# Kernel optimization log

Measured on AMD Instinct MI355X. Metric: run time of the kernel, lower is better.

The kernel has to match this reference:

```python
import jax, jax.numpy as jnp
import numpy as np
from functools import partial

TAU = 2.0
V_TH = 1.0
ALPHA = 2.0  # spikingjelly surrogate.ATan default alpha
EPS = 1e-5   # nn.LayerNorm default eps

@jax.custom_vjp
def atan_spike(v):
    # Heaviside forward; ATan surrogate gradient in bwd.
    return (v >= 0.0).astype(v.dtype)

def _atan_fwd(v):
    return atan_spike(v), v

def _atan_bwd(v, g):
    sg = (ALPHA / 2.0) / (1.0 + (jnp.pi / 2.0 * ALPHA * v) ** 2)
    return (g * sg,)

atan_spike.defvjp(_atan_fwd, _atan_bwd)

def lif_multi_step(x):
    # x: [B, T, H]; LIF with decay_input=True, v_reset=0 (hard reset), detach_reset=True.
    xt = jnp.swapaxes(x, 0, 1)  # [T, B, H]
    v0 = jnp.zeros(x.shape[:1] + x.shape[2:], dtype=x.dtype)  # reset_net per call
    def step(v, x_t):
        v = v + (x_t - v) / TAU            # charge
        s = atan_spike(v - V_TH)           # fire (surrogate grad)
        v = v * (1.0 - jax.lax.stop_gradient(s))  # hard reset to 0, detached spike
        return v, s
    _, spikes = jax.lax.scan(step, v0, xt)
    return jnp.swapaxes(spikes, 0, 1)  # [B, T, H]

def layer_norm(x, gamma, beta):
    mu = jnp.mean(x, axis=-1, keepdims=True)
    var = jnp.mean((x - mu) ** 2, axis=-1, keepdims=True)
    return (x - mu) * jax.lax.rsqrt(var + EPS) * gamma + beta

def setup_inputs() -> dict:
    key = jax.random.key(0)
    ks = jax.random.split(key, 5)
    B, T, D, H = 64, 1024, 256, 512
    x = jax.random.normal(ks[0], (B, T, D), dtype=jnp.float32)
    sc1 = 1.0 / np.sqrt(D)
    sc2 = 1.0 / np.sqrt(H)
    W1 = jax.random.uniform(ks[1], (H, D), jnp.float32, -sc1, sc1)
    b1 = jax.random.uniform(ks[2], (H,), jnp.float32, -sc1, sc1)
    W2 = jax.random.uniform(ks[3], (D, H), jnp.float32, -sc2, sc2)
    b2 = jax.random.uniform(ks[4], (D,), jnp.float32, -sc2, sc2)
    g1 = jnp.ones((H,), jnp.float32); be1 = jnp.zeros((H,), jnp.float32)
    g2 = jnp.ones((D,), jnp.float32); be2 = jnp.zeros((D,), jnp.float32)
    return {"x": x, "W1": W1, "b1": b1, "g1": g1, "be1": be1,
            "W2": W2, "b2": b2, "g2": g2, "be2": be2}

def reference(x, W1, b1, g1, be1, W2, b2, g2, be2):
    residual = x
    h = jnp.einsum('btd,hd->bth', x, W1) + b1   # fc1
    h = layer_norm(h, g1, be1)                   # norm1
    h = lif_multi_step(h)                        # lif1 (dropout = identity, eval)
    y = jnp.einsum('bth,dh->btd', h, W2) + b2    # fc2
    y = layer_norm(y, g2, be2)                   # norm2
    y = lif_multi_step(y)                        # lif2
    return residual + y
```

## Files before the change

kernel.cpp:

```cpp
#include <hip/hip_runtime.h>

typedef int v4i  __attribute__((ext_vector_type(4)));
typedef int v16i __attribute__((ext_vector_type(16)));

#define TT 1024
#define DD 256
#define HH 512
#define CB 32
#define CM (CB*TT)

__device__ __forceinline__ double shfl_xor_d(double x, int m) {
    union { double d; int u[2]; } a; a.d = x;
    a.u[0] = __shfl_xor(a.u[0], m);
    a.u[1] = __shfl_xor(a.u[1], m);
    return a.d;
}

__global__ __launch_bounds__(256) void prep_w_k(const float* __restrict__ W1,
                                                const float* __restrict__ W2,
                                                signed char* __restrict__ W1p,
                                                signed char* __restrict__ W2p) {
    int i = blockIdx.x * 256 + threadIdx.x;
    {
        double a = (double)W1[i];
        double inv = 1024.0, s = 1.0 / 1024.0;
#pragma unroll
        for (int p = 0; p < 5; ++p) {
            int d = (int)(a * inv);
            a -= d * s;
            W1p[(size_t)p * 131072 + i] = (signed char)d;
            inv *= 128.0; s *= (1.0 / 128.0);
        }
    }
    {
        double a = (double)W2[i];
        double inv = 1024.0, s = 1.0 / 1024.0;
#pragma unroll
        for (int p = 0; p < 5; ++p) {
            int d = (int)(a * inv);
            a -= d * s;
            W2p[(size_t)p * 131072 + i] = (signed char)d;
            inv *= 128.0; s *= (1.0 / 128.0);
        }
    }
}

__global__ __launch_bounds__(512, 2) void gemm1_i8(
    const float* __restrict__ X, const signed char* __restrict__ W1p,
    const float* __restrict__ b1, const float* __restrict__ g1,
    const float* __restrict__ be1, double* __restrict__ Hn) {
    __shared__ signed char Asm[5 * 8192];
    __shared__ double RS[8][32], RQ[8][32];
    __shared__ double MUs[32], IVs[32];

    const int tid = threadIdx.x;
    const int wave = tid >> 6, lane = tid & 63, lrow = lane & 31, lhalf = lane >> 5;
    const int m0 = blockIdx.x * 32;

    {
        const int r = tid >> 4;
        const int k0 = (tid & 15) * 16;
        const float* xp = X + (size_t)(m0 + r) * DD + k0;
        float xe[16];
        *(float4*)(xe + 0)  = *(const float4*)(xp + 0);
        *(float4*)(xe + 4)  = *(const float4*)(xp + 4);
        *(float4*)(xe + 8)  = *(const float4*)(xp + 8);
        *(float4*)(xe + 12) = *(const float4*)(xp + 12);
        int pk[5][4];
#pragma unroll
        for (int q = 0; q < 4; ++q)
#pragma unroll
            for (int e = 0; e < 4; ++e) {
                float a = xe[q * 4 + e];
                float inv = 8.0f, s = 0.125f;
#pragma unroll
                for (int p = 0; p < 5; ++p) {
                    int d = (int)(a * inv);
                    a -= (float)d * s;
                    int byte = (d & 255) << (8 * e);
                    if (e == 0) pk[p][q] = byte; else pk[p][q] |= byte;
                    inv *= 128.0f; s *= (1.0f / 128.0f);
                }
            }
        const int swz = k0 ^ ((r & 7) << 4);
#pragma unroll
        for (int p = 0; p < 5; ++p)
            *(v4i*)&Asm[p * 8192 + r * 256 + swz] = *(const v4i*)pk[p];
    }

    v16i acc[5][2];
#pragma unroll
    for (int g = 0; g < 5; ++g)
#pragma unroll
        for (int nt = 0; nt < 2; ++nt)
#pragma unroll
            for (int r = 0; r < 16; ++r) acc[g][nt][r] = 0;

    const signed char* bb[2];
    bb[0] = W1p + (size_t)(wave * 64 + lrow) * 256 + lhalf * 16;
    bb[1] = bb[0] + 32 * 256;

    v4i cb[2][2];
#pragma unroll
    for (int nt = 0; nt < 2; ++nt)
#pragma unroll
        for (int ks = 0; ks < 2; ++ks)
            cb[nt][ks] = *(const v4i*)(bb[nt] + ks * 32);

    __syncthreads();

    const int aswz = (lrow & 7) << 4;
#pragma unroll
    for (int j = 0; j < 5; ++j)
#pragma unroll
        for (int kk = 0; kk < 4; ++kk) {
            const int it = j * 4 + kk;
            v4i nb[2][2];
            if (it < 19) {
                const int nj = (kk == 3) ? j + 1 : j;
                const int nkk = (kk == 3) ? 0 : kk + 1;
                const size_t off = (size_t)nj * 131072 + nkk * 64;
#pragma unroll
                for (int nt = 0; nt < 2; ++nt)
#pragma unroll
                    for (int ks = 0; ks < 2; ++ks)
                        nb[nt][ks] = *(const v4i*)(bb[nt] + off + ks * 32);
            }
#pragma unroll
            for (int i = 0; i + j < 5; ++i) {
                v4i a0 = *(const v4i*)&Asm[i * 8192 + lrow * 256 +
                                           ((kk * 64 + lhalf * 16) ^ aswz)];
                v4i a1 = *(const v4i*)&Asm[i * 8192 + lrow * 256 +
                                           ((kk * 64 + 32 + lhalf * 16) ^ aswz)];
                acc[i + j][0] = __builtin_amdgcn_mfma_i32_32x32x32_i8(a0, cb[0][0], acc[i + j][0], 0, 0, 0);
                acc[i + j][0] = __builtin_amdgcn_mfma_i32_32x32x32_i8(a1, cb[0][1], acc[i + j][0], 0, 0, 0);
                acc[i + j][1] = __builtin_amdgcn_mfma_i32_32x32x32_i8(a0, cb[1][0], acc[i + j][1], 0, 0, 0);
                acc[i + j][1] = __builtin_amdgcn_mfma_i32_32x32x32_i8(a1, cb[1][1], acc[i + j][1], 0, 0, 0);
            }
#pragma unroll
            for (int nt = 0; nt < 2; ++nt)
#pragma unroll
                for (int ks = 0; ks < 2; ++ks)
                    cb[nt][ks] = nb[nt][ks];
        }

    const double scl[5] = {0x1p-13, 0x1p-20, 0x1p-27, 0x1p-34, 0x1p-41};
    double vv[2][16];
    int colc[2];
#pragma unroll
    for (int nt = 0; nt < 2; ++nt) {
        colc[nt] = wave * 64 + nt * 32 + lrow;
        double bcol = (double)b1[colc[nt]];
#pragma unroll
        for (int r = 0; r < 16; ++r) {
            double t = 0.0;
#pragma unroll
            for (int g = 0; g < 5; ++g) t = fma((double)acc[g][nt][r], scl[g], t);
            vv[nt][r] = t + bcol;
        }
    }
    double ps[16], pq[16];
#pragma unroll
    for (int r = 0; r < 16; ++r) {
        ps[r] = vv[0][r] + vv[1][r];
        pq[r] = vv[0][r] * vv[0][r] + vv[1][r] * vv[1][r];
    }
#pragma unroll
    for (int m = 1; m < 32; m <<= 1)
#pragma unroll
        for (int r = 0; r < 16; ++r) {
            ps[r] += shfl_xor_d(ps[r], m);
            pq[r] += shfl_xor_d(pq[r], m);
        }
    if (lrow == 0) {
#pragma unroll
        for (int r = 0; r < 16; ++r) {
            int rw = (r & 3) + 8 * (r >> 2) + 4 * lhalf;
            RS[wave][rw] = ps[r];
            RQ[wave][rw] = pq[r];
        }
    }
    __syncthreads();
    if (tid < 32) {
        double s = 0.0, q = 0.0;
#pragma unroll
        for (int w = 0; w < 8; ++w) { s += RS[w][tid]; q += RQ[w][tid]; }
        double mu = s * (1.0 / 512.0);
        double var = q * (1.0 / 512.0) - mu * mu;
        MUs[tid] = mu;
        IVs[tid] = 1.0 / sqrt(var + 1e-5);
    }
    __syncthreads();
#pragma unroll
    for (int nt = 0; nt < 2; ++nt) {
        int col = colc[nt];
        double gg = (double)g1[col], bb2 = (double)be1[col];
#pragma unroll
        for (int r = 0; r < 16; ++r) {
            int rw = (r & 3) + 8 * (r >> 2) + 4 * lhalf;
            double o = (vv[nt][r] - MUs[rw]) * IVs[rw] * gg + bb2;
            Hn[(size_t)(m0 + rw) * 512 + col] = o;
        }
    }
}

__global__ __launch_bounds__(512, 2) void gemm2_i8(
    const signed char* __restrict__ S, const signed char* __restrict__ W2p,
    const float* __restrict__ b2, const float* __restrict__ g2,
    const float* __restrict__ be2, double* __restrict__ Yn) {
    __shared__ signed char Asm[64 * 512];
    __shared__ double RS[4][64], RQ[4][64];
    __shared__ double MUs[64], IVs[64];

    const int tid = threadIdx.x;
    const int wave = tid >> 6, lane = tid & 63, lrow = lane & 31, lhalf = lane >> 5;
    const int wm = wave >> 2, wn = wave & 3;
    const int m0 = blockIdx.x * 64;

    {
        const int r = tid >> 3, k0 = (tid & 7) * 64;
#pragma unroll
        for (int q = 0; q < 4; ++q) {
            int k = k0 + q * 16;
            v4i v = *(const v4i*)(S + (size_t)(m0 + r) * 512 + k);
            *(v4i*)&Asm[r * 512 + (k ^ ((r & 7) << 4))] = v;
        }
    }

    v16i acc[5][2];
#pragma unroll
    for (int g = 0; g < 5; ++g)
#pragma unroll
        for (int nt = 0; nt < 2; ++nt)
#pragma unroll
            for (int r = 0; r < 16; ++r) acc[g][nt][r] = 0;

    const signed char* bb[2];
    bb[0] = W2p + (size_t)(wn * 64 + lrow) * 512 + lhalf * 16;
    bb[1] = bb[0] + 32 * 512;

    v4i cb[2][4];
#pragma unroll
    for (int nt = 0; nt < 2; ++nt)
#pragma unroll
        for (int ks = 0; ks < 4; ++ks)
            cb[nt][ks] = *(const v4i*)(bb[nt] + ks * 32);

    __syncthreads();

    const int arow = wm * 32 + lrow;
    const int aswz = (arow & 7) << 4;
#pragma unroll
    for (int j = 0; j < 5; ++j)
#pragma unroll
        for (int kk = 0; kk < 4; ++kk) {
            const int it = j * 4 + kk;
            v4i nb[2][4];
            if (it < 19) {
                const int nj = (kk == 3) ? j + 1 : j;
                const int nkk = (kk == 3) ? 0 : kk + 1;
                const size_t off = (size_t)nj * 131072 + nkk * 128;
#pragma unroll
                for (int nt = 0; nt < 2; ++nt)
#pragma unroll
                    for (int ks = 0; ks < 4; ++ks)
                        nb[nt][ks] = *(const v4i*)(bb[nt] + off + ks * 32);
            }
#pragma unroll
            for (int ks = 0; ks < 4; ++ks) {
                v4i a = *(const v4i*)&Asm[arow * 512 +
                                          ((kk * 128 + ks * 32 + lhalf * 16) ^ aswz)];
                acc[j][0] = __builtin_amdgcn_mfma_i32_32x32x32_i8(a, cb[0][ks], acc[j][0], 0, 0, 0);
                acc[j][1] = __builtin_amdgcn_mfma_i32_32x32x32_i8(a, cb[1][ks], acc[j][1], 0, 0, 0);
            }
#pragma unroll
            for (int nt = 0; nt < 2; ++nt)
#pragma unroll
                for (int ks = 0; ks < 4; ++ks)
                    cb[nt][ks] = nb[nt][ks];
        }

    const double scl[5] = {0x1p-10, 0x1p-17, 0x1p-24, 0x1p-31, 0x1p-38};
    double vv[2][16];
    int colc[2];
#pragma unroll
    for (int nt = 0; nt < 2; ++nt) {
        colc[nt] = wn * 64 + nt * 32 + lrow;
        double bcol = (double)b2[colc[nt]];
#pragma unroll
        for (int r = 0; r < 16; ++r) {
            double t = 0.0;
#pragma unroll
            for (int g = 0; g < 5; ++g) t = fma((double)acc[g][nt][r], scl[g], t);
            vv[nt][r] = t + bcol;
        }
    }
    double ps[16], pq[16];
#pragma unroll
    for (int r = 0; r < 16; ++r) {
        ps[r] = vv[0][r] + vv[1][r];
        pq[r] = vv[0][r] * vv[0][r] + vv[1][r] * vv[1][r];
    }
#pragma unroll
    for (int m = 1; m < 32; m <<= 1)
#pragma unroll
        for (int r = 0; r < 16; ++r) {
            ps[r] += shfl_xor_d(ps[r], m);
            pq[r] += shfl_xor_d(pq[r], m);
        }
    if (lrow == 0) {
#pragma unroll
        for (int r = 0; r < 16; ++r) {
            int rw = wm * 32 + (r & 3) + 8 * (r >> 2) + 4 * lhalf;
            RS[wn][rw] = ps[r];
            RQ[wn][rw] = pq[r];
        }
    }
    __syncthreads();
    if (tid < 64) {
        double s = 0.0, q = 0.0;
#pragma unroll
        for (int w = 0; w < 4; ++w) { s += RS[w][tid]; q += RQ[w][tid]; }
        double mu = s * (1.0 / 256.0);
        double var = q * (1.0 / 256.0) - mu * mu;
        MUs[tid] = mu;
        IVs[tid] = 1.0 / sqrt(var + 1e-5);
    }
    __syncthreads();
#pragma unroll
    for (int nt = 0; nt < 2; ++nt) {
        int col = colc[nt];
        double gg = (double)g2[col], bb2 = (double)be2[col];
#pragma unroll
        for (int r = 0; r < 16; ++r) {
            int rw = wm * 32 + (r & 3) + 8 * (r >> 2) + 4 * lhalf;
            double o = (vv[nt][r] - MUs[rw]) * IVs[rw] * gg + bb2;
            Yn[(size_t)(m0 + rw) * 256 + col] = o;
        }
    }
}

__global__ __launch_bounds__(64) void lif1_k(const double* __restrict__ Hn,
                                             signed char* __restrict__ S) {
    int b = blockIdx.x >> 3;
    int h = (blockIdx.x & 7) * 64 + threadIdx.x;
    const double* src = Hn + (size_t)b * TT * HH + h;
    signed char* dst = S + (size_t)b * TT * HH + h;
    double v = 0.0;
    double buf[4][16];
#pragma unroll
    for (int gg = 0; gg < 3; ++gg)
#pragma unroll
        for (int t = 0; t < 16; ++t) buf[gg][t] = src[(size_t)(gg * 16 + t) * HH];
    for (int g4 = 0; g4 < 64; g4 += 4) {
#pragma unroll
        for (int u = 0; u < 4; ++u) {
            int g = g4 + u;
            if (g + 3 < 64) {
#pragma unroll
                for (int t = 0; t < 16; ++t)
                    buf[(u + 3) & 3][t] = src[(size_t)((g + 3) * 16 + t) * HH];
            }
#pragma unroll
            for (int t = 0; t < 16; ++t) {
                v += (buf[u][t] - v) * 0.5;
                bool sp = (v >= 1.0);
                dst[(size_t)(g * 16 + t) * HH] = sp ? 1 : 0;
                if (sp) v = 0.0;
            }
        }
    }
}

__global__ __launch_bounds__(64) void lif2_k(const double* __restrict__ Yn,
                                             const float* __restrict__ X,
                                             float* __restrict__ out) {
    int b = blockIdx.x >> 2;
    int d = (blockIdx.x & 3) * 64 + threadIdx.x;
    const double* src = Yn + (size_t)b * TT * DD + d;
    const float* xs = X + (size_t)b * TT * DD + d;
    float* dst = out + (size_t)b * TT * DD + d;
    double v = 0.0;
    double bufy[4][16];
    float bufx[4][16];
#pragma unroll
    for (int gg = 0; gg < 3; ++gg)
#pragma unroll
        for (int t = 0; t < 16; ++t) {
            bufy[gg][t] = src[(size_t)(gg * 16 + t) * DD];
            bufx[gg][t] = xs[(size_t)(gg * 16 + t) * DD];
        }
    for (int g4 = 0; g4 < 64; g4 += 4) {
#pragma unroll
        for (int u = 0; u < 4; ++u) {
            int g = g4 + u;
            if (g + 3 < 64) {
#pragma unroll
                for (int t = 0; t < 16; ++t) {
                    bufy[(u + 3) & 3][t] = src[(size_t)((g + 3) * 16 + t) * DD];
                    bufx[(u + 3) & 3][t] = xs[(size_t)((g + 3) * 16 + t) * DD];
                }
            }
#pragma unroll
            for (int t = 0; t < 16; ++t) {
                v += (bufy[u][t] - v) * 0.5;
                bool sp = (v >= 1.0);
                dst[(size_t)(g * 16 + t) * DD] = bufx[u][t] + (sp ? 1.0f : 0.0f);
                if (sp) v = 0.0;
            }
        }
    }
}

extern "C" void kernel_launch(void* const* d_in, const int* in_sizes, int n_in,
                              void* d_out, int out_size, void* d_ws, size_t ws_size,
                              hipStream_t stream) {
    const float* x   = (const float*)d_in[0];
    const float* W1  = (const float*)d_in[1];
    const float* b1  = (const float*)d_in[2];
    const float* g1  = (const float*)d_in[3];
    const float* be1 = (const float*)d_in[4];
    const float* W2  = (const float*)d_in[5];
    const float* b2  = (const float*)d_in[6];
    const float* g2  = (const float*)d_in[7];
    const float* be2 = (const float*)d_in[8];
    float* out = (float*)d_out;

    char* ws = (char*)d_ws;
    signed char* W1p = (signed char*)ws;
    signed char* W2p = (signed char*)(ws + (1ull << 20));
    double*      Hn  = (double*)(ws + (2ull << 20));
    signed char* Sb  = (signed char*)(ws + (130ull << 20));
    double*      Yn  = (double*)(ws + (146ull << 20));

    prep_w_k<<<dim3(512), dim3(256), 0, stream>>>(W1, W2, W1p, W2p);

    for (int c = 0; c < 2; ++c) {
        const float* xc = x + (size_t)c * CM * DD;
        float* outc = out + (size_t)c * CM * DD;
        gemm1_i8<<<dim3(CM / 32), dim3(512), 0, stream>>>(xc, W1p, b1, g1, be1, Hn);
        lif1_k<<<dim3(CB * 8), dim3(64), 0, stream>>>(Hn, Sb);
        gemm2_i8<<<dim3(CM / 64), dim3(512), 0, stream>>>(Sb, W2p, b2, g2, be2, Yn);
        lif2_k<<<dim3(CB * 4), dim3(64), 0, stream>>>(Yn, xc, outc);
    }
}
```

Measured before the change: 693.5 us.

## Reorder int8 split-GEMM loops to use one accumulator bank and add nontemporal memory hints

Both int8 split-precision GEMMs are restructured so MFMAs are grouped by output significance level. One pair of v16i accumulators is flushed into double accumulators when each level finishes, replacing five live accumulator banks and aiming to cut VGPR/AGPR pressure. B-fragment prefetch becomes a 3-deep ring two stages ahead. Streaming loads and stores in the GEMMs and LIF kernels become nontemporal, to reduce cache pollution from single-use data. The flushes add int-to-double conversions inside the main loop, which may serialise MFMA issue.

Measured after the change: 1.112 ms. 1.6x slower.

```diff
diff --git a/kernel.cpp b/kernel.cpp
--- a/kernel.cpp
+++ b/kernel.cpp
@@ -1,7 +1,8 @@
 #include <hip/hip_runtime.h>
 
-typedef int v4i  __attribute__((ext_vector_type(4)));
-typedef int v16i __attribute__((ext_vector_type(16)));
+typedef int   v4i __attribute__((ext_vector_type(4)));
+typedef int  v16i __attribute__((ext_vector_type(16)));
+typedef float v4f __attribute__((ext_vector_type(4)));
 
 #define TT 1024
 #define DD 256
@@ -45,6 +46,14 @@
     }
 }
 
+__device__ __forceinline__ void stage1_of(int s, int& g, int& j, int& kk) {
+    if (s < 4)       { g = 0; j = s >> 2;        kk = s & 3; }
+    else if (s < 12) { g = 1; j = (s - 4) >> 2;  kk = (s - 4) & 3; }
+    else if (s < 24) { g = 2; j = (s - 12) >> 2; kk = (s - 12) & 3; }
+    else if (s < 40) { g = 3; j = (s - 24) >> 2; kk = (s - 24) & 3; }
+    else             { g = 4; j = (s - 40) >> 2; kk = (s - 40) & 3; }
+}
+
 __global__ __launch_bounds__(512, 2) void gemm1_i8(
     const float* __restrict__ X, const signed char* __restrict__ W1p,
     const float* __restrict__ b1, const float* __restrict__ g1,
@@ -62,10 +71,10 @@
         const int k0 = (tid & 15) * 16;
         const float* xp = X + (size_t)(m0 + r) * DD + k0;
         float xe[16];
-        *(float4*)(xe + 0)  = *(const float4*)(xp + 0);
-        *(float4*)(xe + 4)  = *(const float4*)(xp + 4);
-        *(float4*)(xe + 8)  = *(const float4*)(xp + 8);
-        *(float4*)(xe + 12) = *(const float4*)(xp + 12);
+        *(v4f*)(xe + 0)  = __builtin_nontemporal_load((const v4f*)(xp + 0));
+        *(v4f*)(xe + 4)  = __builtin_nontemporal_load((const v4f*)(xp + 4));
+        *(v4f*)(xe + 8)  = __builtin_nontemporal_load((const v4f*)(xp + 8));
+        *(v4f*)(xe + 12) = __builtin_nontemporal_load((const v4f*)(xp + 12));
         int pk[5][4];
 #pragma unroll
         for (int q = 0; q < 4; ++q)
@@ -88,76 +97,73 @@
             *(v4i*)&Asm[p * 8192 + r * 256 + swz] = *(const v4i*)pk[p];
     }
 
-    v16i acc[5][2];
-#pragma unroll
-    for (int g = 0; g < 5; ++g)
-#pragma unroll
-        for (int nt = 0; nt < 2; ++nt)
-#pragma unroll
-            for (int r = 0; r < 16; ++r) acc[g][nt][r] = 0;
-
     const signed char* bb[2];
     bb[0] = W1p + (size_t)(wave * 64 + lrow) * 256 + lhalf * 16;
     bb[1] = bb[0] + 32 * 256;
 
-    v4i cb[2][2];
-#pragma unroll
-    for (int nt = 0; nt < 2; ++nt)
-#pragma unroll
-        for (int ks = 0; ks < 2; ++ks)
-            cb[nt][ks] = *(const v4i*)(bb[nt] + ks * 32);
+    v16i bank[2];
+    double vv[2][16];
+#pragma unroll
+    for (int nt = 0; nt < 2; ++nt) {
+#pragma unroll
+        for (int r = 0; r < 16; ++r) { bank[nt][r] = 0; vv[nt][r] = 0.0; }
+    }
+
+    v4i bp[3][2][2];
+#pragma unroll
+    for (int s = 0; s < 2; ++s) {
+        int g, j, kk; stage1_of(s, g, j, kk);
+        const size_t off = (size_t)j * 131072 + kk * 64;
+#pragma unroll
+        for (int nt = 0; nt < 2; ++nt)
+#pragma unroll
+            for (int ks = 0; ks < 2; ++ks)
+                bp[s][nt][ks] = *(const v4i*)(bb[nt] + off + ks * 32);
+    }
 
     __syncthreads();
 
     const int aswz = (lrow & 7) << 4;
-#pragma unroll
-    for (int j = 0; j < 5; ++j)
-#pragma unroll
-        for (int kk = 0; kk < 4; ++kk) {
-            const int it = j * 4 + kk;
-            v4i nb[2][2];
-            if (it < 19) {
-                const int nj = (kk == 3) ? j + 1 : j;
-                const int nkk = (kk == 3) ? 0 : kk + 1;
-                const size_t off = (size_t)nj * 131072 + nkk * 64;
-#pragma unroll
-                for (int nt = 0; nt < 2; ++nt)
-#pragma unroll
-                    for (int ks = 0; ks < 2; ++ks)
-                        nb[nt][ks] = *(const v4i*)(bb[nt] + off + ks * 32);
-            }
-#pragma unroll
-            for (int i = 0; i + j < 5; ++i) {
-                v4i a0 = *(const v4i*)&Asm[i * 8192 + lrow * 256 +
-                                           ((kk * 64 + lhalf * 16) ^ aswz)];
-                v4i a1 = *(const v4i*)&Asm[i * 8192 + lrow * 256 +
-                                           ((kk * 64 + 32 + lhalf * 16) ^ aswz)];
-                acc[i + j][0] = __builtin_amdgcn_mfma_i32_32x32x32_i8(a0, cb[0][0], acc[i + j][0], 0, 0, 0);
-                acc[i + j][0] = __builtin_amdgcn_mfma_i32_32x32x32_i8(a1, cb[0][1], acc[i + j][0], 0, 0, 0);
-                acc[i + j][1] = __builtin_amdgcn_mfma_i32_32x32x32_i8(a0, cb[1][0], acc[i + j][1], 0, 0, 0);
-                acc[i + j][1] = __builtin_amdgcn_mfma_i32_32x32x32_i8(a1, cb[1][1], acc[i + j][1], 0, 0, 0);
-            }
+    const double scl[5] = {0x1p-13, 0x1p-20, 0x1p-27, 0x1p-34, 0x1p-41};
+#pragma unroll
+    for (int s = 0; s < 60; ++s) {
+        int g, j, kk; stage1_of(s, g, j, kk);
+        if (s + 2 < 60) {
+            int g2, j2, k2; stage1_of(s + 2, g2, j2, k2);
+            const size_t off = (size_t)j2 * 131072 + k2 * 64;
 #pragma unroll
             for (int nt = 0; nt < 2; ++nt)
 #pragma unroll
                 for (int ks = 0; ks < 2; ++ks)
-                    cb[nt][ks] = nb[nt][ks];
-        }
-
-    const double scl[5] = {0x1p-13, 0x1p-20, 0x1p-27, 0x1p-34, 0x1p-41};
-    double vv[2][16];
+                    bp[(s + 2) % 3][nt][ks] = *(const v4i*)(bb[nt] + off + ks * 32);
+        }
+        const int i = g - j;
+        v4i a0 = *(const v4i*)&Asm[i * 8192 + lrow * 256 +
+                                   ((kk * 64 + lhalf * 16) ^ aswz)];
+        v4i a1 = *(const v4i*)&Asm[i * 8192 + lrow * 256 +
+                                   ((kk * 64 + 32 + lhalf * 16) ^ aswz)];
+        bank[0] = __builtin_amdgcn_mfma_i32_32x32x32_i8(a0, bp[s % 3][0][0], bank[0], 0, 0, 0);
+        bank[0] = __builtin_amdgcn_mfma_i32_32x32x32_i8(a1, bp[s % 3][0][1], bank[0], 0, 0, 0);
+        bank[1] = __builtin_amdgcn_mfma_i32_32x32x32_i8(a0, bp[s % 3][1][0], bank[1], 0, 0, 0);
+        bank[1] = __builtin_amdgcn_mfma_i32_32x32x32_i8(a1, bp[s % 3][1][1], bank[1], 0, 0, 0);
+        if (kk == 3 && j == g) {
+#pragma unroll
+            for (int nt = 0; nt < 2; ++nt)
+#pragma unroll
+                for (int r = 0; r < 16; ++r) {
+                    vv[nt][r] = fma((double)bank[nt][r], scl[g], vv[nt][r]);
+                    bank[nt][r] = 0;
+                }
+        }
+    }
+
     int colc[2];
 #pragma unroll
     for (int nt = 0; nt < 2; ++nt) {
         colc[nt] = wave * 64 + nt * 32 + lrow;
         double bcol = (double)b1[colc[nt]];
 #pragma unroll
-        for (int r = 0; r < 16; ++r) {
-            double t = 0.0;
-#pragma unroll
-            for (int g = 0; g < 5; ++g) t = fma((double)acc[g][nt][r], scl[g], t);
-            vv[nt][r] = t + bcol;
-        }
+        for (int r = 0; r < 16; ++r) vv[nt][r] += bcol;
     }
     double ps[16], pq[16];
 #pragma unroll
@@ -199,7 +205,7 @@
         for (int r = 0; r < 16; ++r) {
             int rw = (r & 3) + 8 * (r >> 2) + 4 * lhalf;
             double o = (vv[nt][r] - MUs[rw]) * IVs[rw] * gg + bb2;
-            Hn[(size_t)(m0 + rw) * 512 + col] = o;
+            __builtin_nontemporal_store(o, &Hn[(size_t)(m0 + rw) * 512 + col]);
         }
     }
 }
@@ -222,78 +228,75 @@
 #pragma unroll
         for (int q = 0; q < 4; ++q) {
             int k = k0 + q * 16;
-            v4i v = *(const v4i*)(S + (size_t)(m0 + r) * 512 + k);
+            v4i v = __builtin_nontemporal_load(
+                (const v4i*)(S + (size_t)(m0 + r) * 512 + k));
             *(v4i*)&Asm[r * 512 + (k ^ ((r & 7) << 4))] = v;
         }
     }
-
-    v16i acc[5][2];
-#pragma unroll
-    for (int g = 0; g < 5; ++g)
-#pragma unroll
-        for (int nt = 0; nt < 2; ++nt)
-#pragma unroll
-            for (int r = 0; r < 16; ++r) acc[g][nt][r] = 0;
 
     const signed char* bb[2];
     bb[0] = W2p + (size_t)(wn * 64 + lrow) * 512 + lhalf * 16;
     bb[1] = bb[0] + 32 * 512;
 
-    v4i cb[2][4];
-#pragma unroll
-    for (int nt = 0; nt < 2; ++nt)
-#pragma unroll
-        for (int ks = 0; ks < 4; ++ks)
-            cb[nt][ks] = *(const v4i*)(bb[nt] + ks * 32);
+    v16i bank[2];
+    double vv[2][16];
+#pragma unroll
+    for (int nt = 0; nt < 2; ++nt) {
+#pragma unroll
+        for (int r = 0; r < 16; ++r) { bank[nt][r] = 0; vv[nt][r] = 0.0; }
+    }
+
+    v4i bp[3][2][2];
+#pragma unroll
+    for (int s = 0; s < 2; ++s) {
+        const size_t off = (size_t)(s >> 3) * 131072 + (s & 7) * 64;
+#pragma unroll
+        for (int nt = 0; nt < 2; ++nt)
+#pragma unroll
+            for (int ks = 0; ks < 2; ++ks)
+                bp[s][nt][ks] = *(const v4i*)(bb[nt] + off + ks * 32);
+    }
 
     __syncthreads();
 
     const int arow = wm * 32 + lrow;
     const int aswz = (arow & 7) << 4;
-#pragma unroll
-    for (int j = 0; j < 5; ++j)
-#pragma unroll
-        for (int kk = 0; kk < 4; ++kk) {
-            const int it = j * 4 + kk;
-            v4i nb[2][4];
-            if (it < 19) {
-                const int nj = (kk == 3) ? j + 1 : j;
-                const int nkk = (kk == 3) ? 0 : kk + 1;
-                const size_t off = (size_t)nj * 131072 + nkk * 128;
-#pragma unroll
-                for (int nt = 0; nt < 2; ++nt)
-#pragma unroll
-                    for (int ks = 0; ks < 4; ++ks)
-                        nb[nt][ks] = *(const v4i*)(bb[nt] + off + ks * 32);
-            }
-#pragma unroll
-            for (int ks = 0; ks < 4; ++ks) {
-                v4i a = *(const v4i*)&Asm[arow * 512 +
-                                          ((kk * 128 + ks * 32 + lhalf * 16) ^ aswz)];
-                acc[j][0] = __builtin_amdgcn_mfma_i32_32x32x32_i8(a, cb[0][ks], acc[j][0], 0, 0, 0);
-                acc[j][1] = __builtin_amdgcn_mfma_i32_32x32x32_i8(a, cb[1][ks], acc[j][1], 0, 0, 0);
-            }
+    const double scl[5] = {0x1p-10, 0x1p-17, 0x1p-24, 0x1p-31, 0x1p-38};
+#pragma unroll
+    for (int s = 0; s < 40; ++s) {
+        const int j = s >> 3, kh = s & 7;
+        if (s + 2 < 40) {
+            const size_t off = (size_t)((s + 2) >> 3) * 131072 + ((s + 2) & 7) * 64;
 #pragma unroll
             for (int nt = 0; nt < 2; ++nt)
 #pragma unroll
-                for (int ks = 0; ks < 4; ++ks)
-                    cb[nt][ks] = nb[nt][ks];
-        }
-
-    const double scl[5] = {0x1p-10, 0x1p-17, 0x1p-24, 0x1p-31, 0x1p-38};
-    double vv[2][16];
+                for (int ks = 0; ks < 2; ++ks)
+                    bp[(s + 2) % 3][nt][ks] = *(const v4i*)(bb[nt] + off + ks * 32);
+        }
+        v4i a0 = *(const v4i*)&Asm[arow * 512 + ((kh * 64 + lhalf * 16) ^ aswz)];
+        v4i a1 = *(const v4i*)&Asm[arow * 512 + ((kh * 64 + 32 + lhalf * 16) ^ aswz)];
+        bank[0] = __builtin_amdgcn_mfma_i32_32x32x32_i8(a0, bp[s % 3][0][0], bank[0], 0, 0, 0);
+        bank[0] = __builtin_amdgcn_mfma_i32_32x32x32_i8(a1, bp[s % 3][0][1], bank[0], 0, 0, 0);
+        bank[1] = __builtin_amdgcn_mfma_i32_32x32x32_i8(a0, bp[s % 3][1][0], bank[1], 0, 0, 0);
+        bank[1] = __builtin_amdgcn_mfma_i32_32x32x32_i8(a1, bp[s % 3][1][1], bank[1], 0, 0, 0);
+        if (kh == 7) {
+#pragma unroll
+            for (int nt = 0; nt < 2; ++nt)
+#pragma unroll
+                for (int r = 0; r < 16; ++r) {
+                    vv[nt][r] = fma((double)bank[nt][r], scl[j], vv[nt][r]);
+                    bank[nt][r] = 0;
+                }
+        }
+    }
+
     int colc[2];
 #pragma unroll
     for (int nt = 0; nt < 2; ++nt) {
         colc[nt] = wn * 64 + nt * 32 + lrow;
         double bcol = (double)b2[colc[nt]];
 #pragma unroll
-        for (int r = 0; r < 16; ++r) {
-            double t = 0.0;
-#pragma unroll
-            for (int g = 0; g < 5; ++g) t = fma((double)acc[g][nt][r], scl[g], t);
-            vv[nt][r] = t + bcol;
-        }
+        for (int r = 0; r < 16; ++r) vv[nt][r] += bcol;
     }
     double ps[16], pq[16];
 #pragma unroll
@@ -335,7 +338,7 @@
         for (int r = 0; r < 16; ++r) {
             int rw = wm * 32 + (r & 3) + 8 * (r >> 2) + 4 * lhalf;
             double o = (vv[nt][r] - MUs[rw]) * IVs[rw] * gg + bb2;
-            Yn[(size_t)(m0 + rw) * 256 + col] = o;
+            __builtin_nontemporal_store(o, &Yn[(size_t)(m0 + rw) * 256 + col]);
         }
     }
 }
@@ -351,7 +354,8 @@
 #pragma unroll
     for (int gg = 0; gg < 3; ++gg)
 #pragma unroll
-        for (int t = 0; t < 16; ++t) buf[gg][t] = src[(size_t)(gg * 16 + t) * HH];
+        for (int t = 0; t < 16; ++t)
+            buf[gg][t] = __builtin_nontemporal_load(&src[(size_t)(gg * 16 + t) * HH]);
     for (int g4 = 0; g4 < 64; g4 += 4) {
 #pragma unroll
         for (int u = 0; u < 4; ++u) {
@@ -359,7 +363,8 @@
             if (g + 3 < 64) {
 #pragma unroll
                 for (int t = 0; t < 16; ++t)
-                    buf[(u + 3) & 3][t] = src[(size_t)((g + 3) * 16 + t) * HH];
+                    buf[(u + 3) & 3][t] =
+                        __builtin_nontemporal_load(&src[(size_t)((g + 3) * 16 + t) * HH]);
             }
 #pragma unroll
             for (int t = 0; t < 16; ++t) {
@@ -387,8 +392,8 @@
     for (int gg = 0; gg < 3; ++gg)
 #pragma unroll
         for (int t = 0; t < 16; ++t) {
-            bufy[gg][t] = src[(size_t)(gg * 16 + t) * DD];
-            bufx[gg][t] = xs[(size_t)(gg * 16 + t) * DD];
+            bufy[gg][t] = __builtin_nontemporal_load(&src[(size_t)(gg * 16 + t) * DD]);
+            bufx[gg][t] = __builtin_nontemporal_load(&xs[(size_t)(gg * 16 + t) * DD]);
         }
     for (int g4 = 0; g4 < 64; g4 += 4) {
 #pragma unroll
@@ -397,15 +402,18 @@
             if (g + 3 < 64) {
 #pragma unroll
                 for (int t = 0; t < 16; ++t) {
-                    bufy[(u + 3) & 3][t] = src[(size_t)((g + 3) * 16 + t) * DD];
-                    bufx[(u + 3) & 3][t] = xs[(size_t)((g + 3) * 16 + t) * DD];
+                    bufy[(u + 3) & 3][t] =
+                        __builtin_nontemporal_load(&src[(size_t)((g + 3) * 16 + t) * DD]);
+                    bufx[(u + 3) & 3][t] =
+                        __builtin_nontemporal_load(&xs[(size_t)((g + 3) * 16 + t) * DD]);
                 }
             }
 #pragma unroll
             for (int t = 0; t < 16; ++t) {
                 v += (bufy[u][t] - v) * 0.5;
                 bool sp = (v >= 1.0);
-                dst[(size_t)(g * 16 + t) * DD] = bufx[u][t] + (sp ? 1.0f : 0.0f);
+                __builtin_nontemporal_store(bufx[u][t] + (sp ? 1.0f : 0.0f),
+                                            &dst[(size_t)(g * 16 + t) * DD]);
                 if (sp) v = 0.0;
             }
         }
```
